# Optimization experiments

Hardware: AMD Instinct MI355X
Metric: run time of the kernel (lower is better)

## Reference

```python
import jax, jax.numpy as jnp
import numpy as np

B, L, H = 4096, 512, 32  # batch, latent_dim, hidden_size


def setup_inputs() -> dict:
    key = jax.random.key(0)
    ks = jax.random.split(key, 8)
    mu = jax.random.normal(ks[0], (B, L), jnp.float32)
    log_var = jax.random.normal(ks[1], (B, L), jnp.float32)
    eps0 = jax.random.normal(ks[2], (B,), jnp.float32)
    eps = jax.random.normal(ks[3], (B, L), jnp.float32)
    # Per-step MiniSampler params. Sampler idx has in_size = idx+1.
    # Zero-pad first-layer weights to [L, H, L]; row idx only uses cols 0..idx.
    mask = (jnp.arange(L)[None, :] <= jnp.arange(L)[:, None]).astype(jnp.float32)  # [L, L]
    W1 = jax.random.normal(ks[4], (L, H, L), jnp.float32) * 0.1 * mask[:, None, :]
    b1 = jax.random.normal(ks[5], (L, H), jnp.float32) * 0.1
    W2 = jax.random.normal(ks[6], (L, 2, H), jnp.float32) * 0.1
    b2 = jax.random.normal(ks[7], (L, 2), jnp.float32) * 0.1
    return {"mu": mu, "log_var": log_var, "eps0": eps0, "eps": eps,
            "W1": W1, "b1": b1, "W2": W2, "b2": b2}


def reference(mu, log_var, eps0, eps, W1, b1, W2, b2):
    # sample=False path (the default). First latent is reparameterized:
    std0 = jnp.exp(0.5 * log_var[:, 0])
    input0 = eps0 * std0 + mu[:, 0]                      # [B]
    # Input to sampler idx is [input0, mu[:,0], ..., mu[:,idx-1]];
    # W1 is column-masked so one shared padded vector works for all steps.
    v = jnp.concatenate([input0[:, None], mu[:, :-1]], axis=1)  # [B, L]
    h = jax.nn.leaky_relu(jnp.einsum('bj,ihj->bih', v, W1) + b1[None])  # [B, L, H]
    out = jnp.einsum('bih,ioh->bio', h, W2) + b2[None]   # [B, L, 2]
    mus_resampled = out[..., 0]                          # [B, L]
    log_vars_resampled = out[..., 1]                     # [B, L]
    samples = eps * jnp.exp(0.5 * log_vars_resampled) + mus_resampled  # [B, L]
    return (mus_resampled, log_vars_resampled, samples)
```

## Files before the change

### kernel.cpp

```cpp
#include <hip/hip_runtime.h>
#include <hip/hip_bf16.h>

#define Bn 4096
#define Ln 512
#define Hn 32
#define MT 4

using bf16x8 = __attribute__((ext_vector_type(8))) __bf16;
using f32x4  = __attribute__((ext_vector_type(4))) float;

#define GLOAD_LDS16(g, l)                                                          \
  __builtin_amdgcn_global_load_lds(                                                \
      (const __attribute__((address_space(1))) void*)(g),                          \
      (__attribute__((address_space(3))) void*)(l), 16, 0, 0)

__device__ __forceinline__ unsigned short f2bf(float x) {
  unsigned int u = __float_as_uint(x);
  unsigned int r = (u + 0x7FFFu + ((u >> 16) & 1u)) >> 16;
  return (unsigned short)r;
}

__global__ __launch_bounds__(256) void prep_w1_kernel(const float* __restrict__ W1,
                                                      unsigned short* __restrict__ W1b) {
  int idx = blockIdx.x * 256 + threadIdx.x;
  const float4 f = reinterpret_cast<const float4*>(W1)[idx];
  ushort4 o;
  o.x = f2bf(f.x); o.y = f2bf(f.y); o.z = f2bf(f.z); o.w = f2bf(f.w);
  reinterpret_cast<ushort4*>(W1b)[idx] = o;
}

__global__ __launch_bounds__(256) void prep_v_kernel(const float* __restrict__ mu,
                                                     const float* __restrict__ log_var,
                                                     const float* __restrict__ eps0,
                                                     unsigned short* __restrict__ Vb) {
  int idx = blockIdx.x * 256 + threadIdx.x;
  int b = idx >> 9, j = idx & 511;
  float v;
  if (j == 0) {
    v = eps0[b] * expf(0.5f * log_var[(size_t)b * Ln]) + mu[(size_t)b * Ln];
  } else {
    v = mu[(size_t)b * Ln + j - 1];
  }
  Vb[idx] = f2bf(v);
}

__global__ __launch_bounds__(256) void gemm_fused_kernel(
    const unsigned short* __restrict__ Vb,
    const unsigned short* __restrict__ W1b,
    const float* __restrict__ b1,
    const float* __restrict__ W2,
    const float* __restrict__ b2,
    const float* __restrict__ eps,
    float* __restrict__ out)
{
  const int tid  = threadIdx.x;
  const int wid  = tid >> 6;
  const int lane = tid & 63;
  const int l15  = lane & 15;
  const int lq   = lane >> 4;

  const int bid = blockIdx.x;
  const int bn  = 127 - (bid >> 3);
  const int mg  = bid & 7;
  const int mb  = mg * (MT * 128);
  const int nb  = bn * 128;

  const int ksteps = min(8, (bn + 16) >> 4);

  __shared__ unsigned short As[2 * 128 * 64];
  __shared__ unsigned short Bs[2 * 128 * 64];

  const int rowc = lane >> 3;
  const int sswz = (lane & 7) ^ rowc;
  const unsigned short* gA = Vb  + (size_t)(mb + wid * 32 + rowc) * Ln + sswz * 8;
  const unsigned short* gB = W1b + (size_t)(nb + wid * 32 + rowc) * Ln + sswz * 8;
  unsigned short* lA = As + wid * 2048;
  unsigned short* lB = Bs + wid * 2048;

  auto STAGE = [&](int buf, int mt, int k0e) {
    const int    lofs = buf * 8192;
    const size_t ga   = (size_t)mt * (128 * Ln) + k0e;
#pragma unroll
    for (int j = 0; j < 4; ++j) {
      GLOAD_LDS16(gA + ga + (size_t)j * 8 * Ln, lA + lofs + j * 512);
      GLOAD_LDS16(gB + k0e + (size_t)j * 8 * Ln, lB + lofs + j * 512);
    }
  };

  const int arow = (wid >> 1) * 64 + l15;
  const int brow = (wid & 1) * 64 + l15;
  const int swz7 = l15 & 7;

  f32x4 acc[4][4];
#pragma unroll
  for (int fn = 0; fn < 4; ++fn)
#pragma unroll
    for (int fm = 0; fm < 4; ++fm) acc[fn][fm] = f32x4{0.f, 0.f, 0.f, 0.f};

  auto COMPUTE = [&](int buf) {
    const int cofs = buf * 8192;
#pragma unroll
    for (int ks2 = 0; ks2 < 2; ++ks2) {
      const int se = ((ks2 * 4 + lq) ^ swz7) * 8;
      bf16x8 a[4], b[4];
#pragma unroll
      for (int f = 0; f < 4; ++f) {
        a[f] = *reinterpret_cast<const bf16x8*>(As + cofs + (arow + f * 16) * 64 + se);
        b[f] = *reinterpret_cast<const bf16x8*>(Bs + cofs + (brow + f * 16) * 64 + se);
      }
#pragma unroll
      for (int fn = 0; fn < 4; ++fn)
#pragma unroll
        for (int fm = 0; fm < 4; ++fm)
          acc[fn][fm] = __builtin_amdgcn_mfma_f32_16x16x32_bf16(b[fn], a[fm], acc[fn][fm], 0, 0, 0);
    }
  };

  float* mus = out;
  float* lvs = out + (size_t)Bn * Ln;
  float* smp = out + (size_t)2 * Bn * Ln;

  int buf = 0;
  STAGE(0, 0, 0);

  for (int mt = 0; mt < MT; ++mt) {
    for (int k = 0; k < ksteps; ++k) {
      int kn = k + 1, mtn = mt;
      if (kn == ksteps) { kn = 0; ++mtn; }
      if (mtn < MT) {
        STAGE(buf ^ 1, mtn, kn * 64);
        asm volatile("s_waitcnt vmcnt(8)" ::: "memory");
      } else {
        asm volatile("s_waitcnt vmcnt(0)" ::: "memory");
      }
      __builtin_amdgcn_s_barrier();
      __builtin_amdgcn_sched_barrier(0);
      COMPUTE(buf);

      if (k == ksteps - 1) {
        float* S = reinterpret_cast<float*>(Bs + buf * 8192);
        __builtin_amdgcn_s_barrier();

        const int wrow = (wid >> 1) * 64;
#pragma unroll
        for (int il = 0; il < 2; ++il) {
          const int i   = bn * 4 + (wid & 1) * 2 + il;
          const int icl = (wid & 1) * 2 + il;
          float4 b1q[2], w20q[2], w21q[2];
#pragma unroll
          for (int q = 0; q < 2; ++q) {
            const int hb = q * 16 + lq * 4;
            b1q[q]  = *reinterpret_cast<const float4*>(b1 + i * Hn + hb);
            w20q[q] = *reinterpret_cast<const float4*>(W2 + (i * 2 + 0) * Hn + hb);
            w21q[q] = *reinterpret_cast<const float4*>(W2 + (i * 2 + 1) * Hn + hb);
          }
          const float bias0 = b2[i * 2 + 0];
          const float bias1 = b2[i * 2 + 1];
#pragma unroll
          for (int fm = 0; fm < 4; ++fm) {
            float p0 = 0.f, p1 = 0.f;
#pragma unroll
            for (int q = 0; q < 2; ++q) {
              const f32x4& A = acc[il * 2 + q][fm];
              const float* b1f = reinterpret_cast<const float*>(&b1q[q]);
              const float* w0f = reinterpret_cast<const float*>(&w20q[q]);
              const float* w1f = reinterpret_cast<const float*>(&w21q[q]);
#pragma unroll
              for (int r = 0; r < 4; ++r) {
                float x  = A[r] + b1f[r];
                float hv = (x >= 0.f) ? x : 0.01f * x;
                p0 += hv * w0f[r];
                p1 += hv * w1f[r];
              }
            }
            p0 += __shfl_xor(p0, 16);
            p0 += __shfl_xor(p0, 32);
            p1 += __shfl_xor(p1, 16);
            p1 += __shfl_xor(p1, 32);
            if (lq == 0) {
              const int r = wrow + fm * 16 + l15;
              S[icl * 128 + r]       = p0 + bias0;
              S[512 + icl * 128 + r] = p1 + bias1;
            }
          }
        }
        asm volatile("s_waitcnt lgkmcnt(0)" ::: "memory");
        __builtin_amdgcn_s_barrier();

        if (tid < 128) {
          const int    r = tid;
          const size_t o = (size_t)(mb + mt * 128 + r) * Ln + bn * 4;
          float4 muv, lvv;
          muv.x = S[r];       muv.y = S[128 + r]; muv.z = S[256 + r]; muv.w = S[384 + r];
          lvv.x = S[512 + r]; lvv.y = S[640 + r]; lvv.z = S[768 + r]; lvv.w = S[896 + r];
          const float4 ep = *reinterpret_cast<const float4*>(eps + o);
          float4 sm;
          sm.x = ep.x * expf(0.5f * lvv.x) + muv.x;
          sm.y = ep.y * expf(0.5f * lvv.y) + muv.y;
          sm.z = ep.z * expf(0.5f * lvv.z) + muv.z;
          sm.w = ep.w * expf(0.5f * lvv.w) + muv.w;
          *reinterpret_cast<float4*>(mus + o) = muv;
          *reinterpret_cast<float4*>(lvs + o) = lvv;
          *reinterpret_cast<float4*>(smp + o) = sm;
        }
#pragma unroll
        for (int fn = 0; fn < 4; ++fn)
#pragma unroll
          for (int fm = 0; fm < 4; ++fm) acc[fn][fm] = f32x4{0.f, 0.f, 0.f, 0.f};
      }
      __builtin_amdgcn_s_barrier();
      buf ^= 1;
    }
  }
}

extern "C" void kernel_launch(void* const* d_in, const int* in_sizes, int n_in,
                              void* d_out, int out_size, void* d_ws, size_t ws_size,
                              hipStream_t stream) {
  const float* mu      = (const float*)d_in[0];
  const float* log_var = (const float*)d_in[1];
  const float* eps0    = (const float*)d_in[2];
  const float* eps     = (const float*)d_in[3];
  const float* W1      = (const float*)d_in[4];
  const float* b1      = (const float*)d_in[5];
  const float* W2      = (const float*)d_in[6];
  const float* b2      = (const float*)d_in[7];
  float* out = (float*)d_out;

  unsigned short* Vb  = (unsigned short*)d_ws;
  unsigned short* W1b = (unsigned short*)((char*)d_ws + (size_t)Bn * Ln * 2);

  prep_v_kernel<<<(Bn * Ln) / 256, 256, 0, stream>>>(mu, log_var, eps0, Vb);
  prep_w1_kernel<<<(Ln * Hn * Ln) / 4 / 256, 256, 0, stream>>>(W1, W1b);
  gemm_fused_kernel<<<128 * (32 / MT), 256, 0, stream>>>(
      Vb, W1b, b1, W2, b2, eps, out);
}
```

Measured before the change: 85.64 us.

## Skip masked W1 conversion, remap blocks across XCDs, hoist epilogue params

The W1 bf16 conversion kernel now skips float4 groups lying entirely in the zero-masked upper triangle, because the GEMM never reads past k-step bn/16. Block-to-tile mapping is changed so consecutive block IDs on different XCDs get different N tiles, and all blocks sharing an N tile land on the same XCD for L2 reuse of W1. Epilogue b1/W2/b2 loads are hoisted out of the M loop into registers, and leaky-relu and exp are replaced with fmax and exp2. Hoisting adds register pressure.

After: 79.99 us. -6.6%, faster.

```diff
diff --git a/kernel.cpp b/kernel.cpp
--- a/kernel.cpp
+++ b/kernel.cpp
@@ -23,6 +23,10 @@
 __global__ __launch_bounds__(256) void prep_w1_kernel(const float* __restrict__ W1,
                                                       unsigned short* __restrict__ W1b) {
   int idx = blockIdx.x * 256 + threadIdx.x;
+  const int n  = idx >> 7;
+  const int c0 = (idx & 127) * 4;
+  const int i  = n >> 5;
+  if (c0 > i) return;
   const float4 f = reinterpret_cast<const float4*>(W1)[idx];
   ushort4 o;
   o.x = f2bf(f.x); o.y = f2bf(f.y); o.z = f2bf(f.z); o.w = f2bf(f.w);
@@ -60,8 +64,10 @@
   const int lq   = lane >> 4;
 
   const int bid = blockIdx.x;
-  const int bn  = 127 - (bid >> 3);
-  const int mg  = bid & 7;
+  const int xcd = bid & 7;
+  const int s   = bid >> 3;
+  const int bn  = xcd + 8 * (15 - (s >> 3));
+  const int mg  = s & 7;
   const int mb  = mg * (MT * 128);
   const int nb  = bn * 128;
 
@@ -90,6 +96,22 @@
   const int arow = (wid >> 1) * 64 + l15;
   const int brow = (wid & 1) * 64 + l15;
   const int swz7 = l15 & 7;
+
+  float4 b1q[2][2], w20q[2][2], w21q[2][2];
+  float  bias0[2], bias1[2];
+#pragma unroll
+  for (int il = 0; il < 2; ++il) {
+    const int i = bn * 4 + (wid & 1) * 2 + il;
+#pragma unroll
+    for (int q = 0; q < 2; ++q) {
+      const int hb = q * 16 + lq * 4;
+      b1q[il][q]  = *reinterpret_cast<const float4*>(b1 + i * Hn + hb);
+      w20q[il][q] = *reinterpret_cast<const float4*>(W2 + (i * 2 + 0) * Hn + hb);
+      w21q[il][q] = *reinterpret_cast<const float4*>(W2 + (i * 2 + 1) * Hn + hb);
+    }
+    bias0[il] = b2[i * 2 + 0];
+    bias1[il] = b2[i * 2 + 1];
+  }
 
   f32x4 acc[4][4];
 #pragma unroll
@@ -144,31 +166,20 @@
         const int wrow = (wid >> 1) * 64;
 #pragma unroll
         for (int il = 0; il < 2; ++il) {
-          const int i   = bn * 4 + (wid & 1) * 2 + il;
           const int icl = (wid & 1) * 2 + il;
-          float4 b1q[2], w20q[2], w21q[2];
-#pragma unroll
-          for (int q = 0; q < 2; ++q) {
-            const int hb = q * 16 + lq * 4;
-            b1q[q]  = *reinterpret_cast<const float4*>(b1 + i * Hn + hb);
-            w20q[q] = *reinterpret_cast<const float4*>(W2 + (i * 2 + 0) * Hn + hb);
-            w21q[q] = *reinterpret_cast<const float4*>(W2 + (i * 2 + 1) * Hn + hb);
-          }
-          const float bias0 = b2[i * 2 + 0];
-          const float bias1 = b2[i * 2 + 1];
 #pragma unroll
           for (int fm = 0; fm < 4; ++fm) {
             float p0 = 0.f, p1 = 0.f;
 #pragma unroll
             for (int q = 0; q < 2; ++q) {
               const f32x4& A = acc[il * 2 + q][fm];
-              const float* b1f = reinterpret_cast<const float*>(&b1q[q]);
-              const float* w0f = reinterpret_cast<const float*>(&w20q[q]);
-              const float* w1f = reinterpret_cast<const float*>(&w21q[q]);
+              const float* b1f = reinterpret_cast<const float*>(&b1q[il][q]);
+              const float* w0f = reinterpret_cast<const float*>(&w20q[il][q]);
+              const float* w1f = reinterpret_cast<const float*>(&w21q[il][q]);
 #pragma unroll
               for (int r = 0; r < 4; ++r) {
                 float x  = A[r] + b1f[r];
-                float hv = (x >= 0.f) ? x : 0.01f * x;
+                float hv = fmaxf(x, 0.01f * x);
                 p0 += hv * w0f[r];
                 p1 += hv * w1f[r];
               }
@@ -179,8 +190,8 @@
             p1 += __shfl_xor(p1, 32);
             if (lq == 0) {
               const int r = wrow + fm * 16 + l15;
-              S[icl * 128 + r]       = p0 + bias0;
-              S[512 + icl * 128 + r] = p1 + bias1;
+              S[icl * 128 + r]       = p0 + bias0[il];
+              S[512 + icl * 128 + r] = p1 + bias1[il];
             }
           }
         }
@@ -195,10 +206,10 @@
           lvv.x = S[512 + r]; lvv.y = S[640 + r]; lvv.z = S[768 + r]; lvv.w = S[896 + r];
           const float4 ep = *reinterpret_cast<const float4*>(eps + o);
           float4 sm;
-          sm.x = ep.x * expf(0.5f * lvv.x) + muv.x;
-          sm.y = ep.y * expf(0.5f * lvv.y) + muv.y;
-          sm.z = ep.z * expf(0.5f * lvv.z) + muv.z;
-          sm.w = ep.w * expf(0.5f * lvv.w) + muv.w;
+          sm.x = ep.x * __builtin_exp2f(lvv.x * 0.7213475204444817f) + muv.x;
+          sm.y = ep.y * __builtin_exp2f(lvv.y * 0.7213475204444817f) + muv.y;
+          sm.z = ep.z * __builtin_exp2f(lvv.z * 0.7213475204444817f) + muv.z;
+          sm.w = ep.w * __builtin_exp2f(lvv.w * 0.7213475204444817f) + muv.w;
           *reinterpret_cast<float4*>(mus + o) = muv;
           *reinterpret_cast<float4*>(lvs + o) = lvv;
           *reinterpret_cast<float4*>(smp + o) = sm;
```
